# Kernel optimization log

Hardware: AMD Instinct MI355X
Metric: run time of the kernel (lower is better)

## Reference

```python
import jax, jax.numpy as jnp
import numpy as np

H = 16          # num_heads (init kwarg)
EPS = 1e-6      # LayerNorm eps


def rope_freqs(L, d):
    # interleaved RoPE freqs, repeat(f, 'i j -> i (j r)', r=2)
    t = jnp.arange(L, dtype=jnp.float32)
    inv = 1.0 / (10000.0 ** (jnp.arange(0, d, 2, dtype=jnp.float32) / d))
    f = t[:, None] * inv[None, :]          # (L, d//2)
    return jnp.repeat(f, 2, axis=-1)       # (L, d)


def rotate_half(x):
    # pair adjacent elems: (x1, x2) -> (-x2, x1)
    shp = x.shape
    x = x.reshape(shp[:-1] + (shp[-1] // 2, 2))
    x1, x2 = x[..., 0], x[..., 1]
    return jnp.stack((-x2, x1), axis=-1).reshape(shp)


def apply_rope(x, f):
    # x: (B, H, L, d), f: (L, d)
    return x * jnp.cos(f) + rotate_half(x) * jnp.sin(f)


def layernorm(x, g, b):
    m = jnp.mean(x, axis=-1, keepdims=True)
    v = jnp.mean(jnp.square(x - m), axis=-1, keepdims=True)
    return (x - m) * jax.lax.rsqrt(v + EPS) * g + b


def setup_inputs() -> dict:
    key = jax.random.key(0)
    ks = jax.random.split(key, 12)
    B, L, D = 2, 2048, 1024
    Dff = 4 * D
    s = 0.02
    inp = {
        'x': jax.random.normal(ks[0], (B, L, D), jnp.float32),
        'ln1_g': jnp.ones((D,), jnp.float32),
        'ln1_b': jnp.zeros((D,), jnp.float32),
        'wq': jax.random.normal(ks[1], (D, D), jnp.float32) * s,
        'bq': jnp.zeros((D,), jnp.float32),
        'wk': jax.random.normal(ks[2], (D, D), jnp.float32) * s,
        'bk': jnp.zeros((D,), jnp.float32),
        'wv': jax.random.normal(ks[3], (D, D), jnp.float32) * s,
        'bv': jnp.zeros((D,), jnp.float32),
        'wo': jax.random.normal(ks[4], (D, D), jnp.float32) * s,
        'bo': jnp.zeros((D,), jnp.float32),
        'ln2_g': jnp.ones((D,), jnp.float32),
        'ln2_b': jnp.zeros((D,), jnp.float32),
        'w1': jax.random.normal(ks[5], (D, Dff), jnp.float32) * s,
        'b1': jnp.zeros((Dff,), jnp.float32),
        'w2': jax.random.normal(ks[6], (Dff, D), jnp.float32) * s,
        'b2': jnp.zeros((D,), jnp.float32),
        # gates are zero-init in the module; use small random so the block is exercised
        'gate_msa': jax.random.normal(ks[7], (1, 1, D), jnp.float32) * 0.1,
        'gate_mlp': jax.random.normal(ks[8], (1, 1, D), jnp.float32) * 0.1,
    }
    return inp


def reference(x, ln1_g, ln1_b, wq, bq, wk, bk, wv, bv, wo, bo,
              ln2_g, ln2_b, w1, b1, w2, b2, gate_msa, gate_mlp):
    B, L, D = x.shape
    hd = D // H
    # --- self-attention branch ---
    h = layernorm(x, ln1_g, ln1_b)
    q = (h @ wq + bq).reshape(B, L, H, hd).transpose(0, 2, 1, 3)  # (B,H,L,hd)
    k = (h @ wk + bk).reshape(B, L, H, hd).transpose(0, 2, 1, 3)
    v = (h @ wv + bv).reshape(B, L, H, hd).transpose(0, 2, 1, 3)
    f = rope_freqs(L, hd)
    q = apply_rope(q, f)
    k = apply_rope(k, f)
    scores = jnp.einsum('bhic,bhjc->bhij', q, k) / np.float32(np.sqrt(hd))
    attn = jax.nn.softmax(scores, axis=-1)  # dropout disabled (eval)
    o = jnp.einsum('bhij,bhjc->bhic', attn, v)
    o = o.transpose(0, 2, 1, 3).reshape(B, L, D)
    x = x + gate_msa * (o @ wo + bo)
    # --- gated MLP branch ---
    h2 = layernorm(x, ln2_g, ln2_b)
    mlp = jax.nn.gelu(h2 @ w1 + b1, approximate=False) @ w2 + b2
    return x + gate_mlp * mlp
```

## Files before the change

### kernel.cpp

```cpp
#include <hip/hip_runtime.h>

typedef unsigned short u16;
typedef __attribute__((ext_vector_type(4))) float f32x4;
typedef __attribute__((ext_vector_type(8))) short bf16x8;

#define DEV static __device__ __forceinline__

DEV float bf2f(u16 u) { unsigned int i = ((unsigned int)u) << 16; return __builtin_bit_cast(float, i); }
DEV u16 f2bf(float f) {
  unsigned int x = __builtin_bit_cast(unsigned int, f);
  x += 0x7fffu + ((x >> 16) & 1u);
  return (u16)(x >> 16);
}

DEV unsigned cvtpk(float lo, float hi) {
  unsigned r;
  asm("v_cvt_pk_bf16_f32 %0, %1, %2" : "=v"(r) : "v"(lo), "v"(hi));
  return r;
}
DEV float exp2a(float x) {
  float r;
  asm("v_exp_f32 %0, %1" : "=v"(r) : "v"(x));
  return r;
}

template <int N>
DEV void wait_vmcnt() {
  if constexpr (N == 0) asm volatile("s_waitcnt vmcnt(0)" ::: "memory");
  else if constexpr (N == 3) asm volatile("s_waitcnt vmcnt(3)" ::: "memory");
  else if constexpr (N == 4) asm volatile("s_waitcnt vmcnt(4)" ::: "memory");
  else static_assert(N == 0, "unsupported vmcnt");
}

DEV void gload16(const u16* g, u16* l) {
  __builtin_amdgcn_global_load_lds(
      (const __attribute__((address_space(1))) unsigned int*)g,
      (__attribute__((address_space(3))) unsigned int*)l, 16, 0, 0);
}

__global__ __launch_bounds__(256) void ln_k(const float* __restrict__ x,
                                            const float* __restrict__ g,
                                            const float* __restrict__ b,
                                            u16* __restrict__ out) {
  const int row = blockIdx.x;
  const int t = threadIdx.x;
  const float4 v = *(const float4*)(x + (size_t)row * 1024 + t * 4);
  float s = v.x + v.y + v.z + v.w;
  float q = v.x * v.x + v.y * v.y + v.z * v.z + v.w * v.w;
#pragma unroll
  for (int m = 1; m < 64; m <<= 1) { s += __shfl_xor(s, m); q += __shfl_xor(q, m); }
  __shared__ float ss[4], qs[4];
  if ((t & 63) == 0) { ss[t >> 6] = s; qs[t >> 6] = q; }
  __syncthreads();
  s = ss[0] + ss[1] + ss[2] + ss[3];
  q = qs[0] + qs[1] + qs[2] + qs[3];
  const float mean = s * (1.0f / 1024.0f);
  const float var = q * (1.0f / 1024.0f) - mean * mean;
  const float rs = rsqrtf(var + 1e-6f);
  const float4 gv = *(const float4*)(g + t * 4);
  const float4 bv = *(const float4*)(b + t * 4);
  ushort4 o;
  o.x = f2bf((v.x - mean) * rs * gv.x + bv.x);
  o.y = f2bf((v.y - mean) * rs * gv.y + bv.y);
  o.z = f2bf((v.z - mean) * rs * gv.z + bv.z);
  o.w = f2bf((v.w - mean) * rs * gv.w + bv.w);
  *(ushort4*)(out + (size_t)row * 1024 + t * 4) = o;
}

__global__ __launch_bounds__(256) void tcvt_k(const float* __restrict__ src,
                                              u16* __restrict__ dst, int K, int N) {
  __shared__ u16 tl[32][33];
  const int k0 = blockIdx.x * 32, n0 = blockIdx.y * 32;
  const int c = threadIdx.x & 31, r0 = threadIdx.x >> 5;
#pragma unroll
  for (int p = 0; p < 4; p++) {
    const int r = p * 8 + r0;
    tl[r][c] = f2bf(src[(size_t)(k0 + r) * N + n0 + c]);
  }
  __syncthreads();
#pragma unroll
  for (int p = 0; p < 4; p++) {
    const int r = p * 8 + r0;
    dst[(size_t)(n0 + r) * K + k0 + c] = tl[c][r];
  }
}

template <int EPI, int TN>
__global__ __launch_bounds__(256) void gemm_bt(const u16* __restrict__ A,
                                               const u16* __restrict__ Bt,
                                               const float* __restrict__ bias,
                                               const float* __restrict__ resid,
                                               const float* __restrict__ gate,
                                               void* __restrict__ outv,
                                               int M, int N, int K) {
  constexpr int MI = (TN == 128) ? 4 : 2;
  constexpr int WRS = (TN == 128) ? 64 : 32;
  constexpr int L = 2 + TN / 64;
  __shared__ __align__(16) u16 lA[3][128 * 32];
  __shared__ __align__(16) u16 lB[3][TN * 32];
  const int tid = threadIdx.x;
  const int lane = tid & 63, wid = tid >> 6;
  const int l4 = lane >> 4, l15 = lane & 15;
  const int wr = (TN == 128) ? (wid >> 1) : wid;
  const int wc = (TN == 128) ? (wid & 1) : 0;
  const int mBase = blockIdx.x * 128;
  const int nBase = blockIdx.y * TN;

  f32x4 acc[MI][4];
#pragma unroll
  for (int i = 0; i < MI; i++)
#pragma unroll
    for (int j = 0; j < 4; j++)
#pragma unroll
      for (int e = 0; e < 4; e++) acc[i][j][e] = 0.f;

  const int sRow = tid >> 2;
  const int sCol = (tid & 3) * 8;

#define STAGE(bufi, k0)                                                               \
  {                                                                                   \
    _Pragma("unroll") for (int p = 0; p < 2; p++)                                     \
        gload16(A + (size_t)(mBase + p * 64 + sRow) * K + (k0) + sCol,                \
                &lA[bufi][p * 2048 + wid * 512]);                                     \
    _Pragma("unroll") for (int p = 0; p < TN / 64; p++)                               \
        gload16(Bt + (size_t)(nBase + p * 64 + sRow) * K + (k0) + sCol,               \
                &lB[bufi][p * 2048 + wid * 512]);                                     \
  }

  const int nt = K >> 5;
  STAGE(0, 0);
  STAGE(1, 32);
  wait_vmcnt<L>();
  __builtin_amdgcn_s_barrier();
  __builtin_amdgcn_sched_barrier(0);

  int bsel = 0;
  for (int it = 0; it < nt; ++it) {
    bf16x8 af[MI], bfr[4];
#pragma unroll
    for (int mi = 0; mi < MI; mi++)
      af[mi] = *(const bf16x8*)(&lA[bsel][(wr * WRS + mi * 16 + l15) * 32 + l4 * 8]);
#pragma unroll
    for (int ni = 0; ni < 4; ni++)
      bfr[ni] = *(const bf16x8*)(&lB[bsel][(wc * 64 + ni * 16 + l15) * 32 + l4 * 8]);
    if (it + 2 < nt) {
      int b2 = bsel + 2; if (b2 >= 3) b2 -= 3;
      STAGE(b2, (it + 2) * 32);
    }
#pragma unroll
    for (int mi = 0; mi < MI; mi++)
#pragma unroll
      for (int ni = 0; ni < 4; ni++)
        acc[mi][ni] = __builtin_amdgcn_mfma_f32_16x16x32_bf16(af[mi], bfr[ni], acc[mi][ni], 0, 0, 0);
    if (it + 1 < nt) {
      asm volatile("s_waitcnt lgkmcnt(0)" ::: "memory");
      __builtin_amdgcn_sched_barrier(0);
      if (it + 2 < nt) wait_vmcnt<L>();
      else wait_vmcnt<0>();
      __builtin_amdgcn_s_barrier();
      __builtin_amdgcn_sched_barrier(0);
    }
    bsel = (bsel == 2) ? 0 : bsel + 1;
  }
#undef STAGE

  u16* obf = (u16*)outv;
  float* of = (float*)outv;
#pragma unroll
  for (int mi = 0; mi < MI; mi++) {
#pragma unroll
    for (int ni = 0; ni < 4; ni++) {
      const int row0 = mBase + wr * WRS + mi * 16 + l4 * 4;
      const int col = nBase + wc * 64 + ni * 16 + l15;
      const float bb = bias[col];
#pragma unroll
      for (int r = 0; r < 4; r++) {
        const float v = acc[mi][ni][r] + bb;
        const size_t idx = (size_t)(row0 + r) * N + col;
        if (EPI == 0) {
          obf[idx] = f2bf(v);
        } else if (EPI == 1) {
          const float ge = 0.5f * v * (1.0f + erff(v * 0.70710678118654752f));
          obf[idx] = f2bf(ge);
        } else if (EPI == 2) {
          of[idx] = resid[idx] + gate[col] * v;
        } else {
          of[idx] = of[idx] + gate[col] * v;
        }
      }
    }
  }
}

__global__ __launch_bounds__(256) void rope_k(const u16* __restrict__ qkv,
                                              u16* __restrict__ qr, u16* __restrict__ kr) {
  const int sel = blockIdx.y;
  const int rid = blockIdx.x * 8 + (threadIdx.x >> 5);
  const int i = threadIdx.x & 31;
  const int b = rid >> 15;
  const int h = (rid >> 11) & 15;
  const int t = rid & 2047;
  const u16* src = qkv + (size_t)(b * 2048 + t) * 3072 + sel * 1024 + h * 64 + 2 * i;
  const ushort2 uv = *(const ushort2*)src;
  const float x0 = bf2f(uv.x), x1 = bf2f(uv.y);
  const float inv = __expf(-(float)i * 0.28782313662425572f);
  float sn, cs;
  sincosf((float)t * inv, &sn, &cs);
  const float sc = sel ? 1.0f : 0.18033688011112042f;
  ushort2 ov;
  ov.x = f2bf((x0 * cs - x1 * sn) * sc);
  ov.y = f2bf((x1 * cs + x0 * sn) * sc);
  *(ushort2*)((sel ? kr : qr) + (size_t)rid * 64 + 2 * i) = ov;
}

__global__ __launch_bounds__(256) void vtrans_k(const u16* __restrict__ qkv, u16* __restrict__ vt) {
  __shared__ u16 tl[64][65];
  const int bh = blockIdx.x >> 5;
  const int t0 = (blockIdx.x & 31) * 64;
  const int b = bh >> 4, h = bh & 15;
  const int tid = threadIdx.x;
#pragma unroll
  for (int p = 0; p < 16; p++) {
    const int e = p * 256 + tid;
    const int tr = e >> 6, d = e & 63;
    tl[tr][d] = qkv[(size_t)(b * 2048 + t0 + tr) * 3072 + 2048 + h * 64 + d];
  }
  __syncthreads();
#pragma unroll
  for (int p = 0; p < 16; p++) {
    const int e = p * 256 + tid;
    const int dr = e >> 6, tc = e & 63;
    vt[(size_t)(bh * 64 + dr) * 2048 + t0 + tc] = tl[tc][dr];
  }
}

__global__ __launch_bounds__(256) void attn_k(const u16* __restrict__ q,
                                              const u16* __restrict__ k,
                                              const u16* __restrict__ vt,
                                              u16* __restrict__ o) {
  const int bh = blockIdx.y;
  const int tid = threadIdx.x;
  const int wid = tid >> 6, lane = tid & 63;
  const int l4 = lane >> 4, l15 = lane & 15;
  const int qrow0 = blockIdx.x * 128 + wid * 32;

  __shared__ __align__(16) u16 kls[2][4096];
  __shared__ __align__(16) u16 vls[2][4096];
  __shared__ __align__(16) u16 pls[4][2048];
  __shared__ __align__(16) float alds[4][32];

  const size_t qoff = ((size_t)bh * 2048 + qrow0) * 64;
  bf16x8 qf[2][2];
#pragma unroll
  for (int g = 0; g < 2; g++) {
    qf[g][0] = *(const bf16x8*)(q + qoff + (size_t)(g * 16 + l15) * 64 + l4 * 8);
    qf[g][1] = *(const bf16x8*)(q + qoff + (size_t)(g * 16 + l15) * 64 + 32 + l4 * 8);
  }

  float m0 = -1e30f, m1 = -1e30f, ls0 = 0.f, ls1 = 0.f;
  f32x4 oacc[2][4];
#pragma unroll
  for (int g = 0; g < 2; g++)
#pragma unroll
    for (int ni = 0; ni < 4; ni++)
#pragma unroll
      for (int e = 0; e < 4; e++) oacc[g][ni][e] = 0.f;

  const char* kg = (const char*)(k + (size_t)bh * 2048 * 64);
  const char* vg = (const char*)(vt + (size_t)bh * 64 * 2048);
  const int sA = tid, sB = 256 + tid;
  const int rA = sA >> 3, cA = ((sA & 7) ^ (rA & 7)) << 4;
  const int rB = sB >> 3, cB = ((sB & 7) ^ (rB & 7)) << 4;
  u16* kd0 = &kls[0][(size_t)(wid * 64) * 8];
  u16* kd1 = &kls[0][(size_t)(256 + wid * 64) * 8];
  u16* vd0 = &vls[0][(size_t)(wid * 64) * 8];
  u16* vd1 = &vls[0][(size_t)(256 + wid * 64) * 8];

#define STAGE(bufi, kv0)                                                            \
  {                                                                                 \
    const int _o = (bufi)*4096;                                                     \
    gload16((const u16*)(kg + (size_t)((kv0) + rA) * 128 + cA), kd0 + _o);          \
    gload16((const u16*)(kg + (size_t)((kv0) + rB) * 128 + cB), kd1 + _o);          \
    gload16((const u16*)(vg + (size_t)rA * 4096 + (kv0)*2 + cA), vd0 + _o);         \
    gload16((const u16*)(vg + (size_t)rB * 4096 + (kv0)*2 + cB), vd1 + _o);         \
  }

  STAGE(0, 0);
  __syncthreads();

  char* P = (char*)pls[wid];
  float* AL = alds[wid];
  char* prow0 = P + l15 * 128;
  char* prow1 = P + (16 + l15) * 128;
  const int psw = (l15 & 7) << 4;

  int buf = 0;
  for (int it = 0; it < 32; ++it) {
    if (it < 31) STAGE(buf ^ 1, (it + 1) * 64);
    const char* K = (const char*)kls[buf];
    const char* V = (const char*)vls[buf];

    f32x4 s0[4], s1[4];
#pragma unroll
    for (int kt = 0; kt < 4; kt++) {
      const int row = kt * 16 + l15;
      const int sw = (row & 7) << 4;
      const char* kr = K + row * 128;
      const bf16x8 kf0 = *(const bf16x8*)(kr + ((l4 * 16) ^ sw));
      const bf16x8 kf1 = *(const bf16x8*)(kr + ((64 + l4 * 16) ^ sw));
      f32x4 z0 = {0.f, 0.f, 0.f, 0.f}, z1 = {0.f, 0.f, 0.f, 0.f};
      z0 = __builtin_amdgcn_mfma_f32_16x16x32_bf16(kf0, qf[0][0], z0, 0, 0, 0);
      s0[kt] = __builtin_amdgcn_mfma_f32_16x16x32_bf16(kf1, qf[0][1], z0, 0, 0, 0);
      z1 = __builtin_amdgcn_mfma_f32_16x16x32_bf16(kf0, qf[1][0], z1, 0, 0, 0);
      s1[kt] = __builtin_amdgcn_mfma_f32_16x16x32_bf16(kf1, qf[1][1], z1, 0, 0, 0);
    }

    float a00 = fmaxf(fmaxf(s0[0][0], s0[0][1]), fmaxf(s0[0][2], s0[0][3]));
    float a01 = fmaxf(fmaxf(s0[1][0], s0[1][1]), fmaxf(s0[1][2], s0[1][3]));
    float a02 = fmaxf(fmaxf(s0[2][0], s0[2][1]), fmaxf(s0[2][2], s0[2][3]));
    float a03 = fmaxf(fmaxf(s0[3][0], s0[3][1]), fmaxf(s0[3][2], s0[3][3]));
    float pm0 = fmaxf(fmaxf(a00, a01), fmaxf(a02, a03));
    float a10 = fmaxf(fmaxf(s1[0][0], s1[0][1]), fmaxf(s1[0][2], s1[0][3]));
    float a11 = fmaxf(fmaxf(s1[1][0], s1[1][1]), fmaxf(s1[1][2], s1[1][3]));
    float a12 = fmaxf(fmaxf(s1[2][0], s1[2][1]), fmaxf(s1[2][2], s1[2][3]));
    float a13 = fmaxf(fmaxf(s1[3][0], s1[3][1]), fmaxf(s1[3][2], s1[3][3]));
    float pm1 = fmaxf(fmaxf(a10, a11), fmaxf(a12, a13));
    pm0 = fmaxf(pm0, __shfl_xor(pm0, 16));
    pm0 = fmaxf(pm0, __shfl_xor(pm0, 32));
    pm1 = fmaxf(pm1, __shfl_xor(pm1, 16));
    pm1 = fmaxf(pm1, __shfl_xor(pm1, 32));
    const bool need = !__all((pm0 <= m0 + 11.54f) && (pm1 <= m1 + 11.54f));
    float al0 = 1.0f, al1 = 1.0f;
    if (need) {
      const float mn0 = fmaxf(m0, pm0), mn1 = fmaxf(m1, pm1);
      al0 = exp2a(m0 - mn0); al1 = exp2a(m1 - mn1);
      m0 = mn0; m1 = mn1;
      if (l4 == 0) { AL[l15] = al0; AL[16 + l15] = al1; }
    }
#pragma unroll
    for (int kt = 0; kt < 4; kt++)
#pragma unroll
      for (int r = 0; r < 4; r++) {
        s0[kt][r] = exp2a(s0[kt][r] - m0);
        s1[kt][r] = exp2a(s1[kt][r] - m1);
      }
    float e00 = (s0[0][0] + s0[0][1]) + (s0[0][2] + s0[0][3]);
    float e01 = (s0[1][0] + s0[1][1]) + (s0[1][2] + s0[1][3]);
    float e02 = (s0[2][0] + s0[2][1]) + (s0[2][2] + s0[2][3]);
    float e03 = (s0[3][0] + s0[3][1]) + (s0[3][2] + s0[3][3]);
    float ps0 = (e00 + e01) + (e02 + e03);
    float e10 = (s1[0][0] + s1[0][1]) + (s1[0][2] + s1[0][3]);
    float e11 = (s1[1][0] + s1[1][1]) + (s1[1][2] + s1[1][3]);
    float e12 = (s1[2][0] + s1[2][1]) + (s1[2][2] + s1[2][3]);
    float e13 = (s1[3][0] + s1[3][1]) + (s1[3][2] + s1[3][3]);
    float ps1 = (e10 + e11) + (e12 + e13);
    ps0 += __shfl_xor(ps0, 16); ps0 += __shfl_xor(ps0, 32);
    ps1 += __shfl_xor(ps1, 16); ps1 += __shfl_xor(ps1, 32);
    ls0 = ls0 * al0 + ps0;
    ls1 = ls1 * al1 + ps1;

#pragma unroll
    for (int kt = 0; kt < 4; kt++) {
      uint2 w0, w1;
      w0.x = cvtpk(s0[kt][0], s0[kt][1]);
      w0.y = cvtpk(s0[kt][2], s0[kt][3]);
      w1.x = cvtpk(s1[kt][0], s1[kt][1]);
      w1.y = cvtpk(s1[kt][2], s1[kt][3]);
      *(uint2*)(prow0 + ((kt * 32 + l4 * 8) ^ psw)) = w0;
      *(uint2*)(prow1 + ((kt * 32 + l4 * 8) ^ psw)) = w1;
    }
    asm volatile("s_waitcnt lgkmcnt(0)" ::: "memory");
    const bf16x8 pa00 = *(const bf16x8*)(prow0 + ((l4 * 16) ^ psw));
    const bf16x8 pa01 = *(const bf16x8*)(prow0 + ((64 + l4 * 16) ^ psw));
    const bf16x8 pa10 = *(const bf16x8*)(prow1 + ((l4 * 16) ^ psw));
    const bf16x8 pa11 = *(const bf16x8*)(prow1 + ((64 + l4 * 16) ^ psw));
    if (need) {
      const f32x4 a0 = *(const f32x4*)((const char*)AL + l4 * 16);
      const f32x4 a1 = *(const f32x4*)((const char*)AL + 64 + l4 * 16);
#pragma unroll
      for (int ni = 0; ni < 4; ni++) { oacc[0][ni] *= a0; oacc[1][ni] *= a1; }
    }

#pragma unroll
    for (int ni = 0; ni < 4; ni++) {
      const int vrow = ni * 16 + l15;
      const int vsw = (vrow & 7) << 4;
      const char* vr = V + vrow * 128;
      const bf16x8 v0 = *(const bf16x8*)(vr + ((l4 * 16) ^ vsw));
      const bf16x8 v1 = *(const bf16x8*)(vr + ((64 + l4 * 16) ^ vsw));
      oacc[0][ni] = __builtin_amdgcn_mfma_f32_16x16x32_bf16(pa00, v0, oacc[0][ni], 0, 0, 0);
      oacc[0][ni] = __builtin_amdgcn_mfma_f32_16x16x32_bf16(pa01, v1, oacc[0][ni], 0, 0, 0);
      oacc[1][ni] = __builtin_amdgcn_mfma_f32_16x16x32_bf16(pa10, v0, oacc[1][ni], 0, 0, 0);
      oacc[1][ni] = __builtin_amdgcn_mfma_f32_16x16x32_bf16(pa11, v1, oacc[1][ni], 0, 0, 0);
    }
    __syncthreads();
    buf ^= 1;
  }
#undef STAGE

  if (l4 == 0) { AL[l15] = 1.0f / ls0; AL[16 + l15] = 1.0f / ls1; }
  asm volatile("s_waitcnt lgkmcnt(0)" ::: "memory");
  const f32x4 iv0 = *(const f32x4*)((const char*)AL + l4 * 16);
  const f32x4 iv1 = *(const f32x4*)((const char*)AL + 64 + l4 * 16);
  const int b = bh >> 4, h = bh & 15;
#pragma unroll
  for (int g = 0; g < 2; g++) {
#pragma unroll
    for (int r = 0; r < 4; r++) {
      const size_t row = (size_t)b * 2048 + qrow0 + g * 16 + l4 * 4 + r;
      const float iv = g ? iv1[r] : iv0[r];
#pragma unroll
      for (int ni = 0; ni < 4; ni++)
        o[row * 1024 + h * 64 + ni * 16 + l15] = f2bf(oacc[g][ni][r] * iv);
    }
  }
}

extern "C" void kernel_launch(void* const* d_in, const int* in_sizes, int n_in,
                              void* d_out, int out_size, void* d_ws, size_t ws_size,
                              hipStream_t stream) {
  (void)in_sizes; (void)n_in; (void)out_size; (void)ws_size;
  const float* x     = (const float*)d_in[0];
  const float* ln1_g = (const float*)d_in[1];
  const float* ln1_b = (const float*)d_in[2];
  const float* wq    = (const float*)d_in[3];
  const float* bq    = (const float*)d_in[4];
  const float* wk    = (const float*)d_in[5];
  const float* bk    = (const float*)d_in[6];
  const float* wv    = (const float*)d_in[7];
  const float* bv    = (const float*)d_in[8];
  const float* wo    = (const float*)d_in[9];
  const float* bo    = (const float*)d_in[10];
  const float* ln2_g = (const float*)d_in[11];
  const float* ln2_b = (const float*)d_in[12];
  const float* w1    = (const float*)d_in[13];
  const float* b1    = (const float*)d_in[14];
  const float* w2    = (const float*)d_in[15];
  const float* b2    = (const float*)d_in[16];
  const float* gmsa  = (const float*)d_in[17];
  const float* gmlp  = (const float*)d_in[18];
  float* out = (float*)d_out;

  char* w = (char*)d_ws;
  auto alloc = [&](size_t bytes) {
    char* p = w;
    w += (bytes + 255) & ~(size_t)255;
    return p;
  };
  u16* h1     = (u16*)alloc(4096UL * 1024 * 2);
  u16* wqkv_t = (u16*)alloc(3072UL * 1024 * 2);
  u16* wo_t   = (u16*)alloc(1024UL * 1024 * 2);
  u16* w1_t   = (u16*)alloc(4096UL * 1024 * 2);
  u16* w2_t   = (u16*)alloc(1024UL * 4096 * 2);
  float* bqkv = (float*)alloc(3072UL * 4);
  u16* qkv    = (u16*)alloc(4096UL * 3072 * 2);
  u16* q_r    = (u16*)alloc(65536UL * 64 * 2);
  u16* k_r    = (u16*)alloc(65536UL * 64 * 2);
  u16* v_t    = (u16*)alloc(65536UL * 64 * 2);
  u16* o_at   = (u16*)alloc(4096UL * 1024 * 2);
  u16* h2     = (u16*)alloc(4096UL * 1024 * 2);
  u16* g1     = (u16*)alloc(4096UL * 4096 * 2);

  tcvt_k<<<dim3(32, 32), 256, 0, stream>>>(wq, wqkv_t, 1024, 1024);
  tcvt_k<<<dim3(32, 32), 256, 0, stream>>>(wk, wqkv_t + 1024 * 1024, 1024, 1024);
  tcvt_k<<<dim3(32, 32), 256, 0, stream>>>(wv, wqkv_t + 2048 * 1024, 1024, 1024);
  tcvt_k<<<dim3(32, 32), 256, 0, stream>>>(wo, wo_t, 1024, 1024);
  tcvt_k<<<dim3(32, 128), 256, 0, stream>>>(w1, w1_t, 1024, 4096);
  tcvt_k<<<dim3(128, 32), 256, 0, stream>>>(w2, w2_t, 4096, 1024);
  hipMemcpyAsync(bqkv,        bq, 1024 * sizeof(float), hipMemcpyDeviceToDevice, stream);
  hipMemcpyAsync(bqkv + 1024, bk, 1024 * sizeof(float), hipMemcpyDeviceToDevice, stream);
  hipMemcpyAsync(bqkv + 2048, bv, 1024 * sizeof(float), hipMemcpyDeviceToDevice, stream);

  ln_k<<<4096, 256, 0, stream>>>(x, ln1_g, ln1_b, h1);
  gemm_bt<0, 128><<<dim3(32, 24), 256, 0, stream>>>(h1, wqkv_t, bqkv, nullptr, nullptr, qkv, 4096, 3072, 1024);
  rope_k<<<dim3(8192, 2), 256, 0, stream>>>(qkv, q_r, k_r);
  vtrans_k<<<1024, 256, 0, stream>>>(qkv, v_t);
  attn_k<<<dim3(16, 32), 256, 0, stream>>>(q_r, k_r, v_t, o_at);
  gemm_bt<2, 64><<<dim3(32, 16), 256, 0, stream>>>(o_at, wo_t, bo, x, gmsa, out, 4096, 1024, 1024);

  ln_k<<<4096, 256, 0, stream>>>(out, ln2_g, ln2_b, h2);
  gemm_bt<1, 128><<<dim3(32, 32), 256, 0, stream>>>(h2, w1_t, b1, nullptr, nullptr, g1, 4096, 4096, 1024);
  gemm_bt<3, 64><<<dim3(32, 16), 256, 0, stream>>>(g1, w2_t, b2, nullptr, gmlp, out, 4096, 1024, 4096);
}
```

Measured before the change: 289.8 us.

## Swizzle GEMM LDS tiles and halve attention rows per wave for more blocks

The GEMM LDS staging and fragment reads now use an XOR swizzle on the 16-byte column chunk, which is meant to reduce LDS bank conflicts. The attention kernel now handles 16 query rows per wave instead of 32, so the grid doubles to 1024 blocks. Rescale factors are broadcast with shuffles instead of an LDS scratch array. This raises occupancy and parallelism on the device, but each K/V tile loaded into LDS is now reused across half as many query rows, which doubles K/V global traffic.

```diff
diff --git a/kernel.cpp b/kernel.cpp
--- a/kernel.cpp
+++ b/kernel.cpp
@@ -115,7 +115,8 @@
       for (int e = 0; e < 4; e++) acc[i][j][e] = 0.f;
 
   const int sRow = tid >> 2;
-  const int sCol = (tid & 3) * 8;
+  const int sCol = (((tid & 3) ^ ((sRow >> 1) & 3))) * 8;
+  const int rsw = (l15 >> 1) & 3;
 
 #define STAGE(bufi, k0)                                                               \
   {                                                                                   \
@@ -139,10 +140,10 @@
     bf16x8 af[MI], bfr[4];
 #pragma unroll
     for (int mi = 0; mi < MI; mi++)
-      af[mi] = *(const bf16x8*)(&lA[bsel][(wr * WRS + mi * 16 + l15) * 32 + l4 * 8]);
+      af[mi] = *(const bf16x8*)(&lA[bsel][(wr * WRS + mi * 16 + l15) * 32 + (l4 ^ rsw) * 8]);
 #pragma unroll
     for (int ni = 0; ni < 4; ni++)
-      bfr[ni] = *(const bf16x8*)(&lB[bsel][(wc * 64 + ni * 16 + l15) * 32 + l4 * 8]);
+      bfr[ni] = *(const bf16x8*)(&lB[bsel][(wc * 64 + ni * 16 + l15) * 32 + (l4 ^ rsw) * 8]);
     if (it + 2 < nt) {
       int b2 = bsel + 2; if (b2 >= 3) b2 -= 3;
       STAGE(b2, (it + 2) * 32);
@@ -242,29 +243,22 @@
   const int tid = threadIdx.x;
   const int wid = tid >> 6, lane = tid & 63;
   const int l4 = lane >> 4, l15 = lane & 15;
-  const int qrow0 = blockIdx.x * 128 + wid * 32;
+  const int qrow0 = blockIdx.x * 64 + wid * 16;
 
   __shared__ __align__(16) u16 kls[2][4096];
   __shared__ __align__(16) u16 vls[2][4096];
-  __shared__ __align__(16) u16 pls[4][2048];
-  __shared__ __align__(16) float alds[4][32];
+  __shared__ __align__(16) u16 pls[4][1024];
 
   const size_t qoff = ((size_t)bh * 2048 + qrow0) * 64;
-  bf16x8 qf[2][2];
-#pragma unroll
-  for (int g = 0; g < 2; g++) {
-    qf[g][0] = *(const bf16x8*)(q + qoff + (size_t)(g * 16 + l15) * 64 + l4 * 8);
-    qf[g][1] = *(const bf16x8*)(q + qoff + (size_t)(g * 16 + l15) * 64 + 32 + l4 * 8);
-  }
-
-  float m0 = -1e30f, m1 = -1e30f, ls0 = 0.f, ls1 = 0.f;
-  f32x4 oacc[2][4];
-#pragma unroll
-  for (int g = 0; g < 2; g++)
-#pragma unroll
-    for (int ni = 0; ni < 4; ni++)
-#pragma unroll
-      for (int e = 0; e < 4; e++) oacc[g][ni][e] = 0.f;
+  const bf16x8 qf0 = *(const bf16x8*)(q + qoff + (size_t)l15 * 64 + l4 * 8);
+  const bf16x8 qf1 = *(const bf16x8*)(q + qoff + (size_t)l15 * 64 + 32 + l4 * 8);
+
+  float m0 = -1e30f, ls0 = 0.f;
+  f32x4 oacc[4];
+#pragma unroll
+  for (int ni = 0; ni < 4; ni++)
+#pragma unroll
+    for (int e = 0; e < 4; e++) oacc[ni][e] = 0.f;
 
   const char* kg = (const char*)(k + (size_t)bh * 2048 * 64);
   const char* vg = (const char*)(vt + (size_t)bh * 64 * 2048);
@@ -289,9 +283,7 @@
   __syncthreads();
 
   char* P = (char*)pls[wid];
-  float* AL = alds[wid];
   char* prow0 = P + l15 * 128;
-  char* prow1 = P + (16 + l15) * 128;
   const int psw = (l15 & 7) << 4;
 
   int buf = 0;
@@ -300,7 +292,7 @@
     const char* K = (const char*)kls[buf];
     const char* V = (const char*)vls[buf];
 
-    f32x4 s0[4], s1[4];
+    f32x4 s0[4];
 #pragma unroll
     for (int kt = 0; kt < 4; kt++) {
       const int row = kt * 16 + l15;
@@ -308,11 +300,9 @@
       const char* kr = K + row * 128;
       const bf16x8 kf0 = *(const bf16x8*)(kr + ((l4 * 16) ^ sw));
       const bf16x8 kf1 = *(const bf16x8*)(kr + ((64 + l4 * 16) ^ sw));
-      f32x4 z0 = {0.f, 0.f, 0.f, 0.f}, z1 = {0.f, 0.f, 0.f, 0.f};
-      z0 = __builtin_amdgcn_mfma_f32_16x16x32_bf16(kf0, qf[0][0], z0, 0, 0, 0);
-      s0[kt] = __builtin_amdgcn_mfma_f32_16x16x32_bf16(kf1, qf[0][1], z0, 0, 0, 0);
-      z1 = __builtin_amdgcn_mfma_f32_16x16x32_bf16(kf0, qf[1][0], z1, 0, 0, 0);
-      s1[kt] = __builtin_amdgcn_mfma_f32_16x16x32_bf16(kf1, qf[1][1], z1, 0, 0, 0);
+      f32x4 z0 = {0.f, 0.f, 0.f, 0.f};
+      z0 = __builtin_amdgcn_mfma_f32_16x16x32_bf16(kf0, qf0, z0, 0, 0, 0);
+      s0[kt] = __builtin_amdgcn_mfma_f32_16x16x32_bf16(kf1, qf1, z0, 0, 0, 0);
     }
 
     float a00 = fmaxf(fmaxf(s0[0][0], s0[0][1]), fmaxf(s0[0][2], s0[0][3]));
@@ -320,65 +310,44 @@
     float a02 = fmaxf(fmaxf(s0[2][0], s0[2][1]), fmaxf(s0[2][2], s0[2][3]));
     float a03 = fmaxf(fmaxf(s0[3][0], s0[3][1]), fmaxf(s0[3][2], s0[3][3]));
     float pm0 = fmaxf(fmaxf(a00, a01), fmaxf(a02, a03));
-    float a10 = fmaxf(fmaxf(s1[0][0], s1[0][1]), fmaxf(s1[0][2], s1[0][3]));
-    float a11 = fmaxf(fmaxf(s1[1][0], s1[1][1]), fmaxf(s1[1][2], s1[1][3]));
-    float a12 = fmaxf(fmaxf(s1[2][0], s1[2][1]), fmaxf(s1[2][2], s1[2][3]));
-    float a13 = fmaxf(fmaxf(s1[3][0], s1[3][1]), fmaxf(s1[3][2], s1[3][3]));
-    float pm1 = fmaxf(fmaxf(a10, a11), fmaxf(a12, a13));
     pm0 = fmaxf(pm0, __shfl_xor(pm0, 16));
     pm0 = fmaxf(pm0, __shfl_xor(pm0, 32));
-    pm1 = fmaxf(pm1, __shfl_xor(pm1, 16));
-    pm1 = fmaxf(pm1, __shfl_xor(pm1, 32));
-    const bool need = !__all((pm0 <= m0 + 11.54f) && (pm1 <= m1 + 11.54f));
-    float al0 = 1.0f, al1 = 1.0f;
+    const bool need = !__all(pm0 <= m0 + 11.54f);
+    float al0 = 1.0f;
     if (need) {
-      const float mn0 = fmaxf(m0, pm0), mn1 = fmaxf(m1, pm1);
-      al0 = exp2a(m0 - mn0); al1 = exp2a(m1 - mn1);
-      m0 = mn0; m1 = mn1;
-      if (l4 == 0) { AL[l15] = al0; AL[16 + l15] = al1; }
+      const float mn0 = fmaxf(m0, pm0);
+      al0 = exp2a(m0 - mn0);
+      m0 = mn0;
     }
 #pragma unroll
     for (int kt = 0; kt < 4; kt++)
 #pragma unroll
-      for (int r = 0; r < 4; r++) {
-        s0[kt][r] = exp2a(s0[kt][r] - m0);
-        s1[kt][r] = exp2a(s1[kt][r] - m1);
-      }
+      for (int r = 0; r < 4; r++) s0[kt][r] = exp2a(s0[kt][r] - m0);
     float e00 = (s0[0][0] + s0[0][1]) + (s0[0][2] + s0[0][3]);
     float e01 = (s0[1][0] + s0[1][1]) + (s0[1][2] + s0[1][3]);
     float e02 = (s0[2][0] + s0[2][1]) + (s0[2][2] + s0[2][3]);
     float e03 = (s0[3][0] + s0[3][1]) + (s0[3][2] + s0[3][3]);
     float ps0 = (e00 + e01) + (e02 + e03);
-    float e10 = (s1[0][0] + s1[0][1]) + (s1[0][2] + s1[0][3]);
-    float e11 = (s1[1][0] + s1[1][1]) + (s1[1][2] + s1[1][3]);
-    float e12 = (s1[2][0] + s1[2][1]) + (s1[2][2] + s1[2][3]);
-    float e13 = (s1[3][0] + s1[3][1]) + (s1[3][2] + s1[3][3]);
-    float ps1 = (e10 + e11) + (e12 + e13);
-    ps0 += __shfl_xor(ps0, 16); ps0 += __shfl_xor(ps0, 32);
-    ps1 += __shfl_xor(ps1, 16); ps1 += __shfl_xor(ps1, 32);
+    ps0 += __shfl_xor(ps0, 16);
+    ps0 += __shfl_xor(ps0, 32);
     ls0 = ls0 * al0 + ps0;
-    ls1 = ls1 * al1 + ps1;
 
 #pragma unroll
     for (int kt = 0; kt < 4; kt++) {
-      uint2 w0, w1;
+      uint2 w0;
       w0.x = cvtpk(s0[kt][0], s0[kt][1]);
       w0.y = cvtpk(s0[kt][2], s0[kt][3]);
-      w1.x = cvtpk(s1[kt][0], s1[kt][1]);
-      w1.y = cvtpk(s1[kt][2], s1[kt][3]);
       *(uint2*)(prow0 + ((kt * 32 + l4 * 8) ^ psw)) = w0;
-      *(uint2*)(prow1 + ((kt * 32 + l4 * 8) ^ psw)) = w1;
     }
     asm volatile("s_waitcnt lgkmcnt(0)" ::: "memory");
-    const bf16x8 pa00 = *(const bf16x8*)(prow0 + ((l4 * 16) ^ psw));
-    const bf16x8 pa01 = *(const bf16x8*)(prow0 + ((64 + l4 * 16) ^ psw));
-    const bf16x8 pa10 = *(const bf16x8*)(prow1 + ((l4 * 16) ^ psw));
-    const bf16x8 pa11 = *(const bf16x8*)(prow1 + ((64 + l4 * 16) ^ psw));
+    const bf16x8 pa0 = *(const bf16x8*)(prow0 + ((l4 * 16) ^ psw));
+    const bf16x8 pa1 = *(const bf16x8*)(prow0 + ((64 + l4 * 16) ^ psw));
     if (need) {
-      const f32x4 a0 = *(const f32x4*)((const char*)AL + l4 * 16);
-      const f32x4 a1 = *(const f32x4*)((const char*)AL + 64 + l4 * 16);
-#pragma unroll
-      for (int ni = 0; ni < 4; ni++) { oacc[0][ni] *= a0; oacc[1][ni] *= a1; }
+      f32x4 av;
+#pragma unroll
+      for (int r = 0; r < 4; r++) av[r] = __shfl(al0, l4 * 4 + r);
+#pragma unroll
+      for (int ni = 0; ni < 4; ni++) oacc[ni] *= av;
     }
 
 #pragma unroll
@@ -388,31 +357,25 @@
       const char* vr = V + vrow * 128;
       const bf16x8 v0 = *(const bf16x8*)(vr + ((l4 * 16) ^ vsw));
       const bf16x8 v1 = *(const bf16x8*)(vr + ((64 + l4 * 16) ^ vsw));
-      oacc[0][ni] = __builtin_amdgcn_mfma_f32_16x16x32_bf16(pa00, v0, oacc[0][ni], 0, 0, 0);
-      oacc[0][ni] = __builtin_amdgcn_mfma_f32_16x16x32_bf16(pa01, v1, oacc[0][ni], 0, 0, 0);
-      oacc[1][ni] = __builtin_amdgcn_mfma_f32_16x16x32_bf16(pa10, v0, oacc[1][ni], 0, 0, 0);
-      oacc[1][ni] = __builtin_amdgcn_mfma_f32_16x16x32_bf16(pa11, v1, oacc[1][ni], 0, 0, 0);
+      oacc[ni] = __builtin_amdgcn_mfma_f32_16x16x32_bf16(pa0, v0, oacc[ni], 0, 0, 0);
+      oacc[ni] = __builtin_amdgcn_mfma_f32_16x16x32_bf16(pa1, v1, oacc[ni], 0, 0, 0);
     }
     __syncthreads();
     buf ^= 1;
   }
 #undef STAGE
 
-  if (l4 == 0) { AL[l15] = 1.0f / ls0; AL[16 + l15] = 1.0f / ls1; }
-  asm volatile("s_waitcnt lgkmcnt(0)" ::: "memory");
-  const f32x4 iv0 = *(const f32x4*)((const char*)AL + l4 * 16);
-  const f32x4 iv1 = *(const f32x4*)((const char*)AL + 64 + l4 * 16);
+  const float inv0 = 1.0f / ls0;
+  f32x4 iv;
+#pragma unroll
+  for (int r = 0; r < 4; r++) iv[r] = __shfl(inv0, l4 * 4 + r);
   const int b = bh >> 4, h = bh & 15;
 #pragma unroll
-  for (int g = 0; g < 2; g++) {
-#pragma unroll
-    for (int r = 0; r < 4; r++) {
-      const size_t row = (size_t)b * 2048 + qrow0 + g * 16 + l4 * 4 + r;
-      const float iv = g ? iv1[r] : iv0[r];
-#pragma unroll
-      for (int ni = 0; ni < 4; ni++)
-        o[row * 1024 + h * 64 + ni * 16 + l15] = f2bf(oacc[g][ni][r] * iv);
-    }
+  for (int r = 0; r < 4; r++) {
+    const size_t row = (size_t)b * 2048 + qrow0 + l4 * 4 + r;
+#pragma unroll
+    for (int ni = 0; ni < 4; ni++)
+      o[row * 1024 + h * 64 + ni * 16 + l15] = f2bf(oacc[ni][r] * iv[r]);
   }
 }
 
@@ -475,7 +438,7 @@
   gemm_bt<0, 128><<<dim3(32, 24), 256, 0, stream>>>(h1, wqkv_t, bqkv, nullptr, nullptr, qkv, 4096, 3072, 1024);
   rope_k<<<dim3(8192, 2), 256, 0, stream>>>(qkv, q_r, k_r);
   vtrans_k<<<1024, 256, 0, stream>>>(qkv, v_t);
-  attn_k<<<dim3(16, 32), 256, 0, stream>>>(q_r, k_r, v_t, o_at);
+  attn_k<<<dim3(32, 32), 256, 0, stream>>>(q_r, k_r, v_t, o_at);
   gemm_bt<2, 64><<<dim3(32, 16), 256, 0, stream>>>(o_at, wo_t, bo, x, gmsa, out, 4096, 1024, 1024);
 
   ln_k<<<4096, 256, 0, stream>>>(out, ln2_g, ln2_b, h2);
```

Measured after the change: 289.1 us. No clear change (-0.2%).
